# Kernel tuning notes

Hardware: AMD Instinct MI355X
Metric: run time of the kernel (lower is better)

The kernel has to match this reference:

```python
import jax, jax.numpy as jnp
import numpy as np

B, P, E, H, U = 64, 256, 256, 8, 6
HD = E // H            # head_dim = 32
TOPK = 32
DFF = 4 * E
EPS_LN = 1e-5
EPS_RMS = 1.1920929e-07  # torch.finfo(float32).eps (RMSNorm default eps)
NEG = -1e9


def setup_inputs() -> dict:
    key = jax.random.key(0)
    ks = jax.random.split(key, 10)
    s = 0.02
    f32 = jnp.float32
    return {
        "x": jax.random.normal(ks[0], (B, P, E), f32),
        "u": jax.random.normal(ks[1], (B, U, P, P), f32),
        "norm1_w": jnp.ones((E,), f32),
        "norm1_b": jnp.zeros((E,), f32),
        "wq": jax.random.normal(ks[2], (E, E), f32) * s,
        "wk": jax.random.normal(ks[3], (E, E), f32) * s,
        "wv": jax.random.normal(ks[4], (E, E), f32) * s,
        "wo": jax.random.normal(ks[5], (E, E), f32) * s,
        "bo": jnp.zeros((E,), f32),
        "uw": jax.random.normal(ks[6], (H, U), f32) * s,  # 1x1 Conv2d(u_embed->H)
        "ub": jnp.zeros((H,), f32),
        "norm2_w": jnp.ones((E,), f32),
        "norm2_b": jnp.zeros((E,), f32),
        "rms_w": jnp.ones((E,), f32),
        "w1": jax.random.normal(ks[7], (E, DFF), f32) * s,
        "b1": jnp.zeros((DFF,), f32),
        "w2": jax.random.normal(ks[8], (DFF, E), f32) * s,
        "b2": jnp.zeros((E,), f32),
    }


def _layernorm(x, w, b):
    m = jnp.mean(x, axis=-1, keepdims=True)
    v = jnp.mean(jnp.square(x - m), axis=-1, keepdims=True)
    return (x - m) * jax.lax.rsqrt(v + EPS_LN) * w + b


def reference(x, u, norm1_w, norm1_b, wq, wk, wv, wo, bo, uw, ub,
              norm2_w, norm2_b, rms_w, w1, b1, w2, b2):
    xn = _layernorm(x, norm1_w, norm1_b)
    # projections -> [B, H, P, HD]
    q = (xn @ wq).reshape(B, P, H, HD).transpose(0, 2, 1, 3)
    k = (xn @ wk).reshape(B, P, H, HD).transpose(0, 2, 1, 3)
    v = (xn @ wv).reshape(B, P, H, HD).transpose(0, 2, 1, 3)
    scores = jnp.einsum('bhqd,bhkd->bhqk', q, k) * (HD ** -0.5)

    # 1x1 conv bias over pairwise features: [B, U, P, P] -> [B, H, P, P]
    uh = jnp.einsum('bupq,hu->bhpq', u, uw) + ub[None, :, None, None]

    # top-k sparse mask from edge importance (sum of |bias| over heads)
    imp = jnp.abs(uh).sum(axis=1)                    # [B, P, P]
    kk = min(TOPK, P - 1)
    _, idx = jax.lax.top_k(imp, kk)                  # [B, P, kk]
    mask = jnp.zeros((B, P, P), dtype=bool).at[
        jnp.arange(B)[:, None, None],
        jnp.arange(P)[None, :, None],
        idx,
    ].set(True)
    uh = jnp.where(mask[:, None, :, :], uh, NEG)

    attn = jax.nn.softmax(scores + uh, axis=-1)
    attn = jnp.nan_to_num(attn, nan=0.0)

    ctx = jnp.einsum('bhqk,bhkd->bhqd', attn, v)
    ctx = ctx.transpose(0, 2, 1, 3).reshape(B, P, E)
    attn_out = ctx @ wo + bo

    h = _layernorm(attn_out, norm2_w, norm2_b) + x
    hn = h * jax.lax.rsqrt(jnp.mean(h * h, axis=-1, keepdims=True) + EPS_RMS) * rms_w
    z = jax.nn.silu(hn @ w1 + b1) @ w2 + b2
    return z + h, attn
```

## Files before the change

### kernel.cpp

```cpp
#include <hip/hip_runtime.h>
#include <hip/hip_bf16.h>

typedef unsigned short u16;
typedef unsigned long long u64;
typedef __attribute__((ext_vector_type(8))) short short8;
typedef __attribute__((ext_vector_type(4))) float f32x4;

#define NB 64
#define NP 256
#define NE 256
#define NH 8
#define NHD 32
#define NU 6
#define NDFF 1024
#define NM (NB*NP)

__device__ __forceinline__ u16 f2bf(float f) {
  unsigned u = __float_as_uint(f);
  unsigned r = 0x7fffu + ((u >> 16) & 1u);
  return (u16)((u + r) >> 16);
}

__global__ __launch_bounds__(256) void k_prep(
    const float* __restrict__ wq, const float* __restrict__ wk, const float* __restrict__ wv,
    const float* __restrict__ wo, const float* __restrict__ w1, const float* __restrict__ w2,
    u16* __restrict__ wqkvT, u16* __restrict__ woT, u16* __restrict__ w1T, u16* __restrict__ w2T) {
  int tid = blockIdx.x * 256 + threadIdx.x;
  int stride = gridDim.x * 256;
  for (int i = tid; i < 768 * 256; i += stride) {
    int n = i >> 8, kk = i & 255;
    const float* s = (n < 256) ? wq : ((n < 512) ? wk : wv);
    wqkvT[i] = f2bf(s[kk * 256 + (n & 255)]);
  }
  for (int i = tid; i < 256 * 256; i += stride)  { int n = i >> 8,  kk = i & 255;  woT[i] = f2bf(wo[kk * 256 + n]); }
  for (int i = tid; i < 1024 * 256; i += stride) { int n = i >> 8,  kk = i & 255;  w1T[i] = f2bf(w1[kk * 1024 + n]); }
  for (int i = tid; i < 256 * 1024; i += stride) { int n = i >> 10, kk = i & 1023; w2T[i] = f2bf(w2[kk * 256 + n]); }
}

__global__ __launch_bounds__(256) void k_ln1(
    const float* __restrict__ x, const float* __restrict__ w, const float* __restrict__ b,
    u16* __restrict__ xn) {
  int row = blockIdx.x * 4 + (threadIdx.x >> 6);
  int lane = threadIdx.x & 63;
  const float* xr = x + (size_t)row * NE;
  float4 v = *(const float4*)(xr + lane * 4);
  float s = v.x + v.y + v.z + v.w;
  #pragma unroll
  for (int o = 32; o; o >>= 1) s += __shfl_xor(s, o);
  float mean = s * (1.f / 256.f);
  float d0 = v.x - mean, d1 = v.y - mean, d2 = v.z - mean, d3 = v.w - mean;
  float q = d0*d0 + d1*d1 + d2*d2 + d3*d3;
  #pragma unroll
  for (int o = 32; o; o >>= 1) q += __shfl_xor(q, o);
  float r = rsqrtf(q * (1.f / 256.f) + 1e-5f);
  int c = lane * 4;
  ushort4 o4;
  o4.x = f2bf(d0 * r * w[c+0] + b[c+0]);
  o4.y = f2bf(d1 * r * w[c+1] + b[c+1]);
  o4.z = f2bf(d2 * r * w[c+2] + b[c+2]);
  o4.w = f2bf(d3 * r * w[c+3] + b[c+3]);
  *(ushort4*)(xn + (size_t)row * NE + c) = o4;
}

__global__ __launch_bounds__(256) void k_uh(
    const float* __restrict__ u, const float* __restrict__ uw, const float* __restrict__ ub,
    float* __restrict__ uhm) {
  int row = blockIdx.x * 4 + (threadIdx.x >> 6);
  int b = row >> 8, p = row & 255;
  int lane = threadIdx.x & 63;
  double uh[NH][4];
  #pragma unroll
  for (int h = 0; h < NH; h++) {
    double bb = (double)ub[h];
    uh[h][0] = bb; uh[h][1] = bb; uh[h][2] = bb; uh[h][3] = bb;
  }
  #pragma unroll
  for (int uu = 0; uu < NU; uu++) {
    float4 uv = *(const float4*)(u + (((size_t)b * NU + uu) * NP + p) * NP + lane * 4);
    #pragma unroll
    for (int h = 0; h < NH; h++) {
      double w = (double)uw[h * NU + uu];
      uh[h][0] += w * (double)uv.x;
      uh[h][1] += w * (double)uv.y;
      uh[h][2] += w * (double)uv.z;
      uh[h][3] += w * (double)uv.w;
    }
  }
  u64 ib[4];
  #pragma unroll
  for (int i = 0; i < 4; i++) {
    double imp = 0.0;
    #pragma unroll
    for (int h = 0; h < NH; h++) imp += fabs(uh[h][i]);
    ib[i] = (u64)__double_as_longlong(imp);
  }
  u64 res = 0;
  for (int bit = 62; bit >= 0; --bit) {
    u64 cand = res | (1ull << bit);
    int c = __popcll(__ballot(ib[0] >= cand)) + __popcll(__ballot(ib[1] >= cand))
          + __popcll(__ballot(ib[2] >= cand)) + __popcll(__ballot(ib[3] >= cand));
    if (c >= 32) res = cand;
  }
  #pragma unroll
  for (int h = 0; h < NH; h++) {
    float4 o;
    o.x = (ib[0] >= res) ? (float)uh[h][0] : -1e9f;
    o.y = (ib[1] >= res) ? (float)uh[h][1] : -1e9f;
    o.z = (ib[2] >= res) ? (float)uh[h][2] : -1e9f;
    o.w = (ib[3] >= res) ? (float)uh[h][3] : -1e9f;
    *(float4*)(uhm + (((size_t)(b * NH + h)) * NP + p) * NP + lane * 4) = o;
  }
}

__device__ __forceinline__ int lswz(int r, int g) {
  return r * 32 + ((g ^ ((r >> 1) & 3)) << 3);
}

template<class Epi>
__global__ __launch_bounds__(256) void k_gemm(
    const u16* __restrict__ A, const u16* __restrict__ BT, int K, Epi epi) {
  __shared__ __align__(16) u16 As[64 * 32];
  __shared__ __align__(16) u16 Bs[64 * 32];
  int m0 = blockIdx.x * 64, n0 = blockIdx.y * 64;
  int t = threadIdx.x;
  int ar = t >> 2, ag = t & 3;
  const u16* Ap = A + (size_t)(m0 + ar) * K + ag * 8;
  const u16* Bp = BT + (size_t)(n0 + ar) * K + ag * 8;
  int lane = t & 63, wv = t >> 6;
  int fr = lane & 15, fg = lane >> 4;
  int wm = (wv >> 1) * 32, wn = (wv & 1) * 32;
  int sidx = lswz(ar, ag);
  int ia0 = lswz(wm + fr, fg),      ia1 = lswz(wm + 16 + fr, fg);
  int ibx0 = lswz(wn + fr, fg),     ibx1 = lswz(wn + 16 + fr, fg);
  f32x4 acc00 = {0.f,0.f,0.f,0.f}, acc01 = {0.f,0.f,0.f,0.f};
  f32x4 acc10 = {0.f,0.f,0.f,0.f}, acc11 = {0.f,0.f,0.f,0.f};
  for (int k0 = 0; k0 < K; k0 += 32) {
    short8 av = *(const short8*)(Ap + k0);
    short8 bv = *(const short8*)(Bp + k0);
    __syncthreads();
    *(short8*)(As + sidx) = av;
    *(short8*)(Bs + sidx) = bv;
    __syncthreads();
    short8 a0 = *(const short8*)(As + ia0);
    short8 a1 = *(const short8*)(As + ia1);
    short8 b0 = *(const short8*)(Bs + ibx0);
    short8 b1 = *(const short8*)(Bs + ibx1);
    acc00 = __builtin_amdgcn_mfma_f32_16x16x32_bf16(a0, b0, acc00, 0, 0, 0);
    acc01 = __builtin_amdgcn_mfma_f32_16x16x32_bf16(a0, b1, acc01, 0, 0, 0);
    acc10 = __builtin_amdgcn_mfma_f32_16x16x32_bf16(a1, b0, acc10, 0, 0, 0);
    acc11 = __builtin_amdgcn_mfma_f32_16x16x32_bf16(a1, b1, acc11, 0, 0, 0);
  }
  #pragma unroll
  for (int jj = 0; jj < 4; jj++) {
    int mr0 = m0 + wm + fg * 4 + jj, mr1 = mr0 + 16;
    int nc0 = n0 + wn + fr,          nc1 = nc0 + 16;
    epi(mr0, nc0, acc00[jj]);
    epi(mr0, nc1, acc01[jj]);
    epi(mr1, nc0, acc10[jj]);
    epi(mr1, nc1, acc11[jj]);
  }
}

struct EpiQKV {
  u16 *q, *k, *vT;
  __device__ __forceinline__ void operator()(int m, int n, float v) const {
    int b = m >> 8, p = m & 255;
    int h = (n >> 5) & 7, d = n & 31;
    u16 bv = f2bf(v);
    if (n < 256)       q [(((size_t)(b*NH + h)) * NP + p) * NHD + d] = bv;
    else if (n < 512)  k [(((size_t)(b*NH + h)) * NP + p) * NHD + d] = bv;
    else               vT[(((size_t)(b*NH + h)) * NHD + d) * NP + p] = bv;
  }
};
struct EpiWo {
  const float* bo; float* ao;
  __device__ __forceinline__ void operator()(int m, int n, float v) const {
    ao[(size_t)m * NE + n] = v + bo[n];
  }
};
struct EpiFFN1 {
  const float* b1; u16* tb;
  __device__ __forceinline__ void operator()(int m, int n, float v) const {
    float s = v + b1[n];
    tb[(size_t)m * NDFF + n] = f2bf(s / (1.f + __expf(-s)));
  }
};
struct EpiFFN2 {
  const float* b2; const float* hb; float* out0;
  __device__ __forceinline__ void operator()(int m, int n, float v) const {
    out0[(size_t)m * NE + n] = v + b2[n] + hb[(size_t)m * NE + n];
  }
};

__global__ __launch_bounds__(64) void k_attn(
    const u16* __restrict__ qb, const u16* __restrict__ kb, const u16* __restrict__ vTb,
    float* __restrict__ attn, u16* __restrict__ ctx) {
  int bh = blockIdx.x >> 4;
  int r0 = (blockIdx.x & 15) << 4;
  int lane = threadIdx.x;
  int fr = lane & 15, fg = lane >> 4;
  __shared__ __align__(16) float logits[16 * 256];
  __shared__ __align__(16) u16 ps[16 * 256];

  float* uhp = attn + ((size_t)bh * NP + r0) * NP;
  #pragma unroll
  for (int i = 0; i < 16; i++)
    *(float4*)(logits + i * 256 + lane * 4) = *(const float4*)(uhp + i * 256 + lane * 4);

  const u16* qp = qb + ((size_t)bh * NP + r0) * NHD;
  short8 af = *(const short8*)(qp + fr * NHD + fg * 8);
  const u16* kp = kb + (size_t)bh * NP * NHD;
  __syncthreads();
  const float scale = 0.17677669529663687f;
  #pragma unroll
  for (int nb = 0; nb < 16; nb++) {
    short8 bf = *(const short8*)(kp + (nb * 16 + fr) * NHD + fg * 8);
    f32x4 sc = {0.f,0.f,0.f,0.f};
    sc = __builtin_amdgcn_mfma_f32_16x16x32_bf16(af, bf, sc, 0, 0, 0);
    #pragma unroll
    for (int jj = 0; jj < 4; jj++)
      logits[(fg * 4 + jj) * 256 + nb * 16 + fr] += sc[jj] * scale;
  }
  __syncthreads();
  for (int r = 0; r < 16; r++) {
    float v0 = logits[r * 256 + lane];
    float v1 = logits[r * 256 + lane + 64];
    float v2 = logits[r * 256 + lane + 128];
    float v3 = logits[r * 256 + lane + 192];
    float mx = fmaxf(fmaxf(v0, v1), fmaxf(v2, v3));
    #pragma unroll
    for (int o = 32; o; o >>= 1) mx = fmaxf(mx, __shfl_xor(mx, o));
    float e0 = __expf(v0 - mx), e1 = __expf(v1 - mx), e2 = __expf(v2 - mx), e3 = __expf(v3 - mx);
    float s = e0 + e1 + e2 + e3;
    #pragma unroll
    for (int o = 32; o; o >>= 1) s += __shfl_xor(s, o);
    float inv = 1.f / s;
    e0 *= inv; e1 *= inv; e2 *= inv; e3 *= inv;
    float* arow = attn + ((size_t)bh * NP + r0 + r) * NP;
    arow[lane] = e0; arow[lane + 64] = e1; arow[lane + 128] = e2; arow[lane + 192] = e3;
    int rs = r & 7;
    int c0 = lane, c1 = lane + 64, c2 = lane + 128, c3 = lane + 192;
    ps[r * 256 + (((c0 >> 3) ^ rs) << 3) + (c0 & 7)] = f2bf(e0);
    ps[r * 256 + (((c1 >> 3) ^ rs) << 3) + (c1 & 7)] = f2bf(e1);
    ps[r * 256 + (((c2 >> 3) ^ rs) << 3) + (c2 & 7)] = f2bf(e2);
    ps[r * 256 + (((c3 >> 3) ^ rs) << 3) + (c3 & 7)] = f2bf(e3);
  }
  __syncthreads();
  const u16* vp = vTb + (size_t)bh * NHD * NP;
  f32x4 c0a = {0.f,0.f,0.f,0.f}, c1a = {0.f,0.f,0.f,0.f};
  #pragma unroll
  for (int kk = 0; kk < 8; kk++) {
    int cc = kk * 32 + fg * 8;
    short8 pa  = *(const short8*)(ps + fr * 256 + (((kk * 4 + fg) ^ (fr & 7)) << 3));
    short8 vb0 = *(const short8*)(vp + fr * NP + cc);
    short8 vb1 = *(const short8*)(vp + (16 + fr) * NP + cc);
    c0a = __builtin_amdgcn_mfma_f32_16x16x32_bf16(pa, vb0, c0a, 0, 0, 0);
    c1a = __builtin_amdgcn_mfma_f32_16x16x32_bf16(pa, vb1, c1a, 0, 0, 0);
  }
  int b = bh >> 3, h = bh & 7;
  #pragma unroll
  for (int jj = 0; jj < 4; jj++) {
    int prow = r0 + fg * 4 + jj;
    u16* crow = ctx + ((size_t)(b * NP + prow)) * NE + h * NHD;
    crow[fr]      = f2bf(c0a[jj]);
    crow[16 + fr] = f2bf(c1a[jj]);
  }
}

__global__ __launch_bounds__(256) void k_ln2rms(
    const float* __restrict__ ao, const float* __restrict__ x,
    const float* __restrict__ w, const float* __restrict__ b, const float* __restrict__ rw,
    float* __restrict__ hbuf, u16* __restrict__ hn) {
  int row = blockIdx.x * 4 + (threadIdx.x >> 6);
  int lane = threadIdx.x & 63;
  float4 v = *(const float4*)(ao + (size_t)row * NE + lane * 4);
  float s = v.x + v.y + v.z + v.w;
  #pragma unroll
  for (int o = 32; o; o >>= 1) s += __shfl_xor(s, o);
  float mean = s * (1.f / 256.f);
  float d0 = v.x - mean, d1 = v.y - mean, d2 = v.z - mean, d3 = v.w - mean;
  float q = d0*d0 + d1*d1 + d2*d2 + d3*d3;
  #pragma unroll
  for (int o = 32; o; o >>= 1) q += __shfl_xor(q, o);
  float r = rsqrtf(q * (1.f / 256.f) + 1e-5f);
  float4 xv = *(const float4*)(x + (size_t)row * NE + lane * 4);
  int c = lane * 4;
  float h0 = d0 * r * w[c+0] + b[c+0] + xv.x;
  float h1 = d1 * r * w[c+1] + b[c+1] + xv.y;
  float h2 = d2 * r * w[c+2] + b[c+2] + xv.z;
  float h3 = d3 * r * w[c+3] + b[c+3] + xv.w;
  *(float4*)(hbuf + (size_t)row * NE + c) = make_float4(h0, h1, h2, h3);
  float ss = h0*h0 + h1*h1 + h2*h2 + h3*h3;
  #pragma unroll
  for (int o = 32; o; o >>= 1) ss += __shfl_xor(ss, o);
  float rm = rsqrtf(ss * (1.f / 256.f) + 1.1920929e-07f);
  ushort4 o4;
  o4.x = f2bf(h0 * rm * rw[c+0]);
  o4.y = f2bf(h1 * rm * rw[c+1]);
  o4.z = f2bf(h2 * rm * rw[c+2]);
  o4.w = f2bf(h3 * rm * rw[c+3]);
  *(ushort4*)(hn + (size_t)row * NE + c) = o4;
}

extern "C" void kernel_launch(void* const* d_in, const int* in_sizes, int n_in,
                              void* d_out, int out_size, void* d_ws, size_t ws_size,
                              hipStream_t stream) {
  (void)in_sizes; (void)n_in; (void)out_size; (void)ws_size;
  const float* x    = (const float*)d_in[0];
  const float* u    = (const float*)d_in[1];
  const float* n1w  = (const float*)d_in[2];
  const float* n1b  = (const float*)d_in[3];
  const float* wq   = (const float*)d_in[4];
  const float* wk   = (const float*)d_in[5];
  const float* wv   = (const float*)d_in[6];
  const float* wo   = (const float*)d_in[7];
  const float* bo   = (const float*)d_in[8];
  const float* uw   = (const float*)d_in[9];
  const float* ub   = (const float*)d_in[10];
  const float* n2w  = (const float*)d_in[11];
  const float* n2b  = (const float*)d_in[12];
  const float* rmsw = (const float*)d_in[13];
  const float* w1   = (const float*)d_in[14];
  const float* b1   = (const float*)d_in[15];
  const float* w2   = (const float*)d_in[16];
  const float* b2   = (const float*)d_in[17];
  float* out0 = (float*)d_out;
  float* attn = out0 + (size_t)NM * NE;
  char* ws = (char*)d_ws;
  u16* wqkvT = (u16*)(ws + 0x000000);
  u16* woT   = (u16*)(ws + 0x060000);
  u16* w1T   = (u16*)(ws + 0x080000);
  u16* w2T   = (u16*)(ws + 0x100000);
  u16* qb    = (u16*)(ws + 0x200000);
  u16* kb    = (u16*)(ws + 0xA00000);
  u16* vTb   = (u16*)(ws + 0x1200000);
  u16* xn    = (u16*)(ws + 0x1A00000);
  u16* ctx   = (u16*)(ws + 0x2200000);
  float* ao  = (float*)(ws + 0x2A00000);
  float* hb  = (float*)(ws + 0x3A00000);
  u16* hn    = (u16*)(ws + 0x4A00000);
  u16* tb    = (u16*)(ws + 0x200000);

  k_prep<<<dim3(256), dim3(256), 0, stream>>>(wq, wk, wv, wo, w1, w2, wqkvT, woT, w1T, w2T);
  k_ln1<<<dim3(NM/4), dim3(256), 0, stream>>>(x, n1w, n1b, xn);
  k_uh<<<dim3(NM/4), dim3(256), 0, stream>>>(u, uw, ub, attn);
  k_gemm<<<dim3(NM/64, 768/64), dim3(256), 0, stream>>>(xn, wqkvT, NE, EpiQKV{qb, kb, vTb});
  k_attn<<<dim3(NB*NH*16), dim3(64), 0, stream>>>(qb, kb, vTb, attn, ctx);
  k_gemm<<<dim3(NM/64, NE/64), dim3(256), 0, stream>>>(ctx, woT, NE, EpiWo{bo, ao});
  k_ln2rms<<<dim3(NM/4), dim3(256), 0, stream>>>(ao, x, n2w, n2b, rmsw, hb, hn);
  k_gemm<<<dim3(NM/64, NDFF/64), dim3(256), 0, stream>>>(hn, w1T, NE, EpiFFN1{b1, tb});
  k_gemm<<<dim3(NM/64, NE/64), dim3(256), 0, stream>>>(tb, w2T, NDFF, EpiFFN2{b2, hb, out0});
}
```

Measured before the change: 487.3 us.

## Fuse bias/top-k mask into attention and switch to 128x128 direct-to-LDS GEMM

Removes the separate bias kernel that wrote the masked fp32 bias into the attention output buffer. The per-head conv bias and top-k mask are now computed inside a fused attention kernel, one block per (batch, 16-row tile) with a wave per head, and stored as bf16 in LDS. This avoids the round trip of a large fp32 tensor through global memory. Softmax now runs in registers on MFMA fragments. All GEMMs move to 128x128 tiles with 4x4 MFMA per wave, loading global memory straight to LDS. The risks are bf16 rounding of the bias, unswizzled LDS reads that may cause bank conflicts, and fewer blocks for the smaller GEMMs.

```diff
diff --git a/kernel.cpp b/kernel.cpp
--- a/kernel.cpp
+++ b/kernel.cpp
@@ -19,6 +19,16 @@
   unsigned u = __float_as_uint(f);
   unsigned r = 0x7fffu + ((u >> 16) & 1u);
   return (u16)((u + r) >> 16);
+}
+__device__ __forceinline__ float bf2f(u16 v) {
+  unsigned u = ((unsigned)v) << 16;
+  return __uint_as_float(u);
+}
+
+__device__ __forceinline__ void gl_lds16(const u16* g, u16* l) {
+  __builtin_amdgcn_global_load_lds(
+      (const __attribute__((address_space(1))) unsigned int*)g,
+      (__attribute__((address_space(3))) unsigned int*)l, 16, 0, 0);
 }
 
 __global__ __launch_bounds__(256) void k_prep(
@@ -62,103 +72,46 @@
   *(ushort4*)(xn + (size_t)row * NE + c) = o4;
 }
 
-__global__ __launch_bounds__(256) void k_uh(
-    const float* __restrict__ u, const float* __restrict__ uw, const float* __restrict__ ub,
-    float* __restrict__ uhm) {
-  int row = blockIdx.x * 4 + (threadIdx.x >> 6);
-  int b = row >> 8, p = row & 255;
-  int lane = threadIdx.x & 63;
-  double uh[NH][4];
-  #pragma unroll
-  for (int h = 0; h < NH; h++) {
-    double bb = (double)ub[h];
-    uh[h][0] = bb; uh[h][1] = bb; uh[h][2] = bb; uh[h][3] = bb;
-  }
-  #pragma unroll
-  for (int uu = 0; uu < NU; uu++) {
-    float4 uv = *(const float4*)(u + (((size_t)b * NU + uu) * NP + p) * NP + lane * 4);
-    #pragma unroll
-    for (int h = 0; h < NH; h++) {
-      double w = (double)uw[h * NU + uu];
-      uh[h][0] += w * (double)uv.x;
-      uh[h][1] += w * (double)uv.y;
-      uh[h][2] += w * (double)uv.z;
-      uh[h][3] += w * (double)uv.w;
-    }
-  }
-  u64 ib[4];
-  #pragma unroll
-  for (int i = 0; i < 4; i++) {
-    double imp = 0.0;
-    #pragma unroll
-    for (int h = 0; h < NH; h++) imp += fabs(uh[h][i]);
-    ib[i] = (u64)__double_as_longlong(imp);
-  }
-  u64 res = 0;
-  for (int bit = 62; bit >= 0; --bit) {
-    u64 cand = res | (1ull << bit);
-    int c = __popcll(__ballot(ib[0] >= cand)) + __popcll(__ballot(ib[1] >= cand))
-          + __popcll(__ballot(ib[2] >= cand)) + __popcll(__ballot(ib[3] >= cand));
-    if (c >= 32) res = cand;
-  }
-  #pragma unroll
-  for (int h = 0; h < NH; h++) {
-    float4 o;
-    o.x = (ib[0] >= res) ? (float)uh[h][0] : -1e9f;
-    o.y = (ib[1] >= res) ? (float)uh[h][1] : -1e9f;
-    o.z = (ib[2] >= res) ? (float)uh[h][2] : -1e9f;
-    o.w = (ib[3] >= res) ? (float)uh[h][3] : -1e9f;
-    *(float4*)(uhm + (((size_t)(b * NH + h)) * NP + p) * NP + lane * 4) = o;
-  }
-}
-
-__device__ __forceinline__ int lswz(int r, int g) {
-  return r * 32 + ((g ^ ((r >> 1) & 3)) << 3);
-}
-
 template<class Epi>
-__global__ __launch_bounds__(256) void k_gemm(
+__global__ __launch_bounds__(256, 4) void k_gemm128(
     const u16* __restrict__ A, const u16* __restrict__ BT, int K, Epi epi) {
-  __shared__ __align__(16) u16 As[64 * 32];
-  __shared__ __align__(16) u16 Bs[64 * 32];
-  int m0 = blockIdx.x * 64, n0 = blockIdx.y * 64;
-  int t = threadIdx.x;
-  int ar = t >> 2, ag = t & 3;
-  const u16* Ap = A + (size_t)(m0 + ar) * K + ag * 8;
-  const u16* Bp = BT + (size_t)(n0 + ar) * K + ag * 8;
-  int lane = t & 63, wv = t >> 6;
-  int fr = lane & 15, fg = lane >> 4;
-  int wm = (wv >> 1) * 32, wn = (wv & 1) * 32;
-  int sidx = lswz(ar, ag);
-  int ia0 = lswz(wm + fr, fg),      ia1 = lswz(wm + 16 + fr, fg);
-  int ibx0 = lswz(wn + fr, fg),     ibx1 = lswz(wn + 16 + fr, fg);
-  f32x4 acc00 = {0.f,0.f,0.f,0.f}, acc01 = {0.f,0.f,0.f,0.f};
-  f32x4 acc10 = {0.f,0.f,0.f,0.f}, acc11 = {0.f,0.f,0.f,0.f};
+  __shared__ __align__(16) u16 As[128 * 32];
+  __shared__ __align__(16) u16 Bs[128 * 32];
+  const int t = threadIdx.x;
+  const int m0 = blockIdx.x * 128, n0 = blockIdx.y * 128;
+  const int lane = t & 63, wv = t >> 6;
+  const int fr = lane & 15, fg = lane >> 4;
+  const int wm = (wv >> 1) * 64, wn = (wv & 1) * 64;
+  const u16* Ap = A + (size_t)(m0 + (t >> 2)) * K + (t & 3) * 8;
+  const u16* Bp = BT + (size_t)(n0 + (t >> 2)) * K + (t & 3) * 8;
+  u16* lA = As + wv * 512;
+  u16* lB = Bs + wv * 512;
+  f32x4 acc[4][4] = {};
   for (int k0 = 0; k0 < K; k0 += 32) {
-    short8 av = *(const short8*)(Ap + k0);
-    short8 bv = *(const short8*)(Bp + k0);
     __syncthreads();
-    *(short8*)(As + sidx) = av;
-    *(short8*)(Bs + sidx) = bv;
+    gl_lds16(Ap + k0, lA);
+    gl_lds16(Ap + k0 + (size_t)64 * K, lA + 2048);
+    gl_lds16(Bp + k0, lB);
+    gl_lds16(Bp + k0 + (size_t)64 * K, lB + 2048);
     __syncthreads();
-    short8 a0 = *(const short8*)(As + ia0);
-    short8 a1 = *(const short8*)(As + ia1);
-    short8 b0 = *(const short8*)(Bs + ibx0);
-    short8 b1 = *(const short8*)(Bs + ibx1);
-    acc00 = __builtin_amdgcn_mfma_f32_16x16x32_bf16(a0, b0, acc00, 0, 0, 0);
-    acc01 = __builtin_amdgcn_mfma_f32_16x16x32_bf16(a0, b1, acc01, 0, 0, 0);
-    acc10 = __builtin_amdgcn_mfma_f32_16x16x32_bf16(a1, b0, acc10, 0, 0, 0);
-    acc11 = __builtin_amdgcn_mfma_f32_16x16x32_bf16(a1, b1, acc11, 0, 0, 0);
-  }
-  #pragma unroll
-  for (int jj = 0; jj < 4; jj++) {
-    int mr0 = m0 + wm + fg * 4 + jj, mr1 = mr0 + 16;
-    int nc0 = n0 + wn + fr,          nc1 = nc0 + 16;
-    epi(mr0, nc0, acc00[jj]);
-    epi(mr0, nc1, acc01[jj]);
-    epi(mr1, nc0, acc10[jj]);
-    epi(mr1, nc1, acc11[jj]);
-  }
+    short8 a[4], b[4];
+    #pragma unroll
+    for (int i = 0; i < 4; i++) a[i] = *(const short8*)(As + (wm + i * 16 + fr) * 32 + fg * 8);
+    #pragma unroll
+    for (int j = 0; j < 4; j++) b[j] = *(const short8*)(Bs + (wn + j * 16 + fr) * 32 + fg * 8);
+    #pragma unroll
+    for (int i = 0; i < 4; i++)
+      #pragma unroll
+      for (int j = 0; j < 4; j++)
+        acc[i][j] = __builtin_amdgcn_mfma_f32_16x16x32_bf16(a[i], b[j], acc[i][j], 0, 0, 0);
+  }
+  #pragma unroll
+  for (int i = 0; i < 4; i++)
+    #pragma unroll
+    for (int j = 0; j < 4; j++)
+      #pragma unroll
+      for (int jj = 0; jj < 4; jj++)
+        epi(m0 + wm + i * 16 + fg * 4 + jj, n0 + wn + j * 16 + fr, acc[i][j][jj]);
 }
 
 struct EpiQKV {
@@ -192,78 +145,135 @@
   }
 };
 
-__global__ __launch_bounds__(64) void k_attn(
+__global__ __launch_bounds__(512, 4) void k_fattn(
+    const float* __restrict__ u, const float* __restrict__ uw, const float* __restrict__ ub,
     const u16* __restrict__ qb, const u16* __restrict__ kb, const u16* __restrict__ vTb,
     float* __restrict__ attn, u16* __restrict__ ctx) {
-  int bh = blockIdx.x >> 4;
-  int r0 = (blockIdx.x & 15) << 4;
-  int lane = threadIdx.x;
-  int fr = lane & 15, fg = lane >> 4;
-  __shared__ __align__(16) float logits[16 * 256];
-  __shared__ __align__(16) u16 ps[16 * 256];
-
-  float* uhp = attn + ((size_t)bh * NP + r0) * NP;
-  #pragma unroll
-  for (int i = 0; i < 16; i++)
-    *(float4*)(logits + i * 256 + lane * 4) = *(const float4*)(uhp + i * 256 + lane * 4);
-
-  const u16* qp = qb + ((size_t)bh * NP + r0) * NHD;
+  __shared__ __align__(16) u16 bias[NH * 16 * 256];
+  const int b = blockIdx.x >> 4;
+  const int r0 = (blockIdx.x & 15) << 4;
+  const int w = threadIdx.x >> 6;
+  const int lane = threadIdx.x & 63;
+  const int fr = lane & 15, fg = lane >> 4;
+  const u16 NEGBF = f2bf(-1e9f);
+
+  for (int rr = 0; rr < 2; rr++) {
+    const int p = r0 + 2 * w + rr;
+    const float* up = u + ((size_t)b * NU * NP + p) * NP + lane * 4;
+    double uh[NH][4];
+    #pragma unroll
+    for (int h = 0; h < NH; h++) {
+      double bb = (double)ub[h];
+      uh[h][0] = bb; uh[h][1] = bb; uh[h][2] = bb; uh[h][3] = bb;
+    }
+    #pragma unroll
+    for (int uu = 0; uu < NU; uu++) {
+      float4 uv = *(const float4*)(up + (size_t)uu * (NP * NP));
+      #pragma unroll
+      for (int h = 0; h < NH; h++) {
+        double ww = (double)uw[h * NU + uu];
+        uh[h][0] += ww * (double)uv.x;
+        uh[h][1] += ww * (double)uv.y;
+        uh[h][2] += ww * (double)uv.z;
+        uh[h][3] += ww * (double)uv.w;
+      }
+    }
+    u64 ib[4];
+    #pragma unroll
+    for (int i = 0; i < 4; i++) {
+      double imp = 0.0;
+      #pragma unroll
+      for (int h = 0; h < NH; h++) imp += fabs(uh[h][i]);
+      ib[i] = (u64)__double_as_longlong(imp);
+    }
+    u64 res = 0;
+    for (int bit = 62; bit >= 0; --bit) {
+      u64 cand = res | (1ull << bit);
+      int c = __popcll(__ballot(ib[0] >= cand)) + __popcll(__ballot(ib[1] >= cand))
+            + __popcll(__ballot(ib[2] >= cand)) + __popcll(__ballot(ib[3] >= cand));
+      if (c >= 32) res = cand;
+    }
+    const int rl = 2 * w + rr;
+    #pragma unroll
+    for (int h = 0; h < NH; h++) {
+      ushort4 o;
+      o.x = (ib[0] >= res) ? f2bf((float)uh[h][0]) : NEGBF;
+      o.y = (ib[1] >= res) ? f2bf((float)uh[h][1]) : NEGBF;
+      o.z = (ib[2] >= res) ? f2bf((float)uh[h][2]) : NEGBF;
+      o.w = (ib[3] >= res) ? f2bf((float)uh[h][3]) : NEGBF;
+      *(ushort4*)(bias + (h * 16 + rl) * 256 + lane * 4) = o;
+    }
+  }
+  __syncthreads();
+
+  const size_t bh = (size_t)b * NH + w;
+  const u16* qp = qb + (bh * NP + r0) * NHD;
   short8 af = *(const short8*)(qp + fr * NHD + fg * 8);
-  const u16* kp = kb + (size_t)bh * NP * NHD;
-  __syncthreads();
+  const u16* kp = kb + bh * NP * NHD;
   const float scale = 0.17677669529663687f;
+  f32x4 sc[16];
   #pragma unroll
   for (int nb = 0; nb < 16; nb++) {
-    short8 bf = *(const short8*)(kp + (nb * 16 + fr) * NHD + fg * 8);
-    f32x4 sc = {0.f,0.f,0.f,0.f};
-    sc = __builtin_amdgcn_mfma_f32_16x16x32_bf16(af, bf, sc, 0, 0, 0);
+    short8 bfr = *(const short8*)(kp + (nb * 16 + fr) * NHD + fg * 8);
+    f32x4 z = {0.f, 0.f, 0.f, 0.f};
+    z = __builtin_amdgcn_mfma_f32_16x16x32_bf16(af, bfr, z, 0, 0, 0);
     #pragma unroll
     for (int jj = 0; jj < 4; jj++)
-      logits[(fg * 4 + jj) * 256 + nb * 16 + fr] += sc[jj] * scale;
-  }
-  __syncthreads();
-  for (int r = 0; r < 16; r++) {
-    float v0 = logits[r * 256 + lane];
-    float v1 = logits[r * 256 + lane + 64];
-    float v2 = logits[r * 256 + lane + 128];
-    float v3 = logits[r * 256 + lane + 192];
-    float mx = fmaxf(fmaxf(v0, v1), fmaxf(v2, v3));
-    #pragma unroll
-    for (int o = 32; o; o >>= 1) mx = fmaxf(mx, __shfl_xor(mx, o));
-    float e0 = __expf(v0 - mx), e1 = __expf(v1 - mx), e2 = __expf(v2 - mx), e3 = __expf(v3 - mx);
-    float s = e0 + e1 + e2 + e3;
-    #pragma unroll
-    for (int o = 32; o; o >>= 1) s += __shfl_xor(s, o);
-    float inv = 1.f / s;
-    e0 *= inv; e1 *= inv; e2 *= inv; e3 *= inv;
-    float* arow = attn + ((size_t)bh * NP + r0 + r) * NP;
-    arow[lane] = e0; arow[lane + 64] = e1; arow[lane + 128] = e2; arow[lane + 192] = e3;
-    int rs = r & 7;
-    int c0 = lane, c1 = lane + 64, c2 = lane + 128, c3 = lane + 192;
-    ps[r * 256 + (((c0 >> 3) ^ rs) << 3) + (c0 & 7)] = f2bf(e0);
-    ps[r * 256 + (((c1 >> 3) ^ rs) << 3) + (c1 & 7)] = f2bf(e1);
-    ps[r * 256 + (((c2 >> 3) ^ rs) << 3) + (c2 & 7)] = f2bf(e2);
-    ps[r * 256 + (((c3 >> 3) ^ rs) << 3) + (c3 & 7)] = f2bf(e3);
-  }
-  __syncthreads();
-  const u16* vp = vTb + (size_t)bh * NHD * NP;
-  f32x4 c0a = {0.f,0.f,0.f,0.f}, c1a = {0.f,0.f,0.f,0.f};
+      sc[nb][jj] = z[jj] * scale + bf2f(bias[(w * 16 + fg * 4 + jj) * 256 + nb * 16 + fr]);
+  }
+  float mx[4] = {-1e30f, -1e30f, -1e30f, -1e30f};
+  #pragma unroll
+  for (int nb = 0; nb < 16; nb++)
+    #pragma unroll
+    for (int jj = 0; jj < 4; jj++) mx[jj] = fmaxf(mx[jj], sc[nb][jj]);
+  #pragma unroll
+  for (int o = 1; o < 16; o <<= 1)
+    #pragma unroll
+    for (int jj = 0; jj < 4; jj++) mx[jj] = fmaxf(mx[jj], __shfl_xor(mx[jj], o));
+  float sum[4] = {0.f, 0.f, 0.f, 0.f};
+  #pragma unroll
+  for (int nb = 0; nb < 16; nb++)
+    #pragma unroll
+    for (int jj = 0; jj < 4; jj++) {
+      sc[nb][jj] = __expf(sc[nb][jj] - mx[jj]);
+      sum[jj] += sc[nb][jj];
+    }
+  #pragma unroll
+  for (int o = 1; o < 16; o <<= 1)
+    #pragma unroll
+    for (int jj = 0; jj < 4; jj++) sum[jj] += __shfl_xor(sum[jj], o);
+  float inv[4];
+  #pragma unroll
+  for (int jj = 0; jj < 4; jj++) inv[jj] = 1.f / sum[jj];
+
+  float* ap = attn + (bh * NP + r0 + fg * 4) * NP;
+  u16* ps = bias + w * 4096;
+  #pragma unroll
+  for (int nb = 0; nb < 16; nb++)
+    #pragma unroll
+    for (int jj = 0; jj < 4; jj++) {
+      float e = sc[nb][jj] * inv[jj];
+      ap[jj * 256 + nb * 16 + fr] = e;
+      int row = fg * 4 + jj, col = nb * 16 + fr;
+      ps[row * 256 + ((((col >> 3) ^ (row & 7)) << 3) | (col & 7))] = f2bf(e);
+    }
+
+  const u16* vp = vTb + bh * NHD * NP;
+  f32x4 c0 = {0.f, 0.f, 0.f, 0.f}, c1 = {0.f, 0.f, 0.f, 0.f};
   #pragma unroll
   for (int kk = 0; kk < 8; kk++) {
-    int cc = kk * 32 + fg * 8;
-    short8 pa  = *(const short8*)(ps + fr * 256 + (((kk * 4 + fg) ^ (fr & 7)) << 3));
-    short8 vb0 = *(const short8*)(vp + fr * NP + cc);
-    short8 vb1 = *(const short8*)(vp + (16 + fr) * NP + cc);
-    c0a = __builtin_amdgcn_mfma_f32_16x16x32_bf16(pa, vb0, c0a, 0, 0, 0);
-    c1a = __builtin_amdgcn_mfma_f32_16x16x32_bf16(pa, vb1, c1a, 0, 0, 0);
-  }
-  int b = bh >> 3, h = bh & 7;
+    short8 pa = *(const short8*)(ps + fr * 256 + (((kk * 4 + fg) ^ (fr & 7)) << 3));
+    short8 v0 = *(const short8*)(vp + fr * NP + kk * 32 + fg * 8);
+    short8 v1 = *(const short8*)(vp + (16 + fr) * NP + kk * 32 + fg * 8);
+    c0 = __builtin_amdgcn_mfma_f32_16x16x32_bf16(pa, v0, c0, 0, 0, 0);
+    c1 = __builtin_amdgcn_mfma_f32_16x16x32_bf16(pa, v1, c1, 0, 0, 0);
+  }
   #pragma unroll
   for (int jj = 0; jj < 4; jj++) {
     int prow = r0 + fg * 4 + jj;
-    u16* crow = ctx + ((size_t)(b * NP + prow)) * NE + h * NHD;
-    crow[fr]      = f2bf(c0a[jj]);
-    crow[16 + fr] = f2bf(c1a[jj]);
+    u16* crow = ctx + ((size_t)(b * NP + prow)) * NE + w * NHD;
+    crow[fr]      = f2bf(c0[jj]);
+    crow[16 + fr] = f2bf(c1[jj]);
   }
 }
 
@@ -343,11 +353,10 @@
 
   k_prep<<<dim3(256), dim3(256), 0, stream>>>(wq, wk, wv, wo, w1, w2, wqkvT, woT, w1T, w2T);
   k_ln1<<<dim3(NM/4), dim3(256), 0, stream>>>(x, n1w, n1b, xn);
-  k_uh<<<dim3(NM/4), dim3(256), 0, stream>>>(u, uw, ub, attn);
-  k_gemm<<<dim3(NM/64, 768/64), dim3(256), 0, stream>>>(xn, wqkvT, NE, EpiQKV{qb, kb, vTb});
-  k_attn<<<dim3(NB*NH*16), dim3(64), 0, stream>>>(qb, kb, vTb, attn, ctx);
-  k_gemm<<<dim3(NM/64, NE/64), dim3(256), 0, stream>>>(ctx, woT, NE, EpiWo{bo, ao});
+  k_gemm128<<<dim3(NM/128, 768/128), dim3(256), 0, stream>>>(xn, wqkvT, NE, EpiQKV{qb, kb, vTb});
+  k_fattn<<<dim3(NB*16), dim3(512), 0, stream>>>(u, uw, ub, qb, kb, vTb, attn, ctx);
+  k_gemm128<<<dim3(NM/128, NE/128), dim3(256), 0, stream>>>(ctx, woT, NE, EpiWo{bo, ao});
   k_ln2rms<<<dim3(NM/4), dim3(256), 0, stream>>>(ao, x, n2w, n2b, rmsw, hb, hn);
-  k_gemm<<<dim3(NM/64, NDFF/64), dim3(256), 0, stream>>>(hn, w1T, NE, EpiFFN1{b1, tb});
-  k_gemm<<<dim3(NM/64, NE/64), dim3(256), 0, stream>>>(tb, w2T, NDFF, EpiFFN2{b2, hb, out0});
-}
+  k_gemm128<<<dim3(NM/128, NDFF/128), dim3(256), 0, stream>>>(hn, w1T, NE, EpiFFN1{b1, tb});
+  k_gemm128<<<dim3(NM/128, NE/128), dim3(256), 0, stream>>>(tb, w2T, NDFF, EpiFFN2{b2, hb, out0});
+}
```

Result: no change. 480.7 us (-1.4%).
